# Performance work log

Measured on AMD Instinct MI355X. Metric: run time of the kernel, lower is better.

Reference implementation:

```python
import jax, jax.numpy as jnp
import numpy as np

K = 1024
HEADS = 16


def setup_inputs() -> dict:
    key = jax.random.key(0)
    ks = jax.random.split(key, 6)
    x = jax.random.normal(ks[0], (2, 2048, K), dtype=jnp.float32)
    sc = 1.0 / np.sqrt(K)
    Wq = jax.random.normal(ks[1], (K, K), dtype=jnp.float32) * sc
    Wk = jax.random.normal(ks[2], (K, K), dtype=jnp.float32) * sc
    Wv = jax.random.normal(ks[3], (K, K), dtype=jnp.float32) * sc
    Wu = jax.random.normal(ks[4], (K, K), dtype=jnp.float32) * sc
    bu = jax.random.normal(ks[5], (K,), dtype=jnp.float32) * 0.01
    return {"x": x, "Wq": Wq, "Wk": Wk, "Wv": Wv, "Wu": Wu, "bu": bu}


def reference(x, Wq, Wk, Wv, Wu, bu):
    b, t, k = x.shape
    h = HEADS
    s = k // h
    # torch Linear: y = x @ W.T
    q = (x @ Wq.T).reshape(b, t, h, s)
    kk = (x @ Wk.T).reshape(b, t, h, s)
    v = (x @ Wv.T).reshape(b, t, h, s)
    # NOTE: original scales by sqrt(k) (full model dim), not sqrt(head dim)
    dot = jnp.einsum('bqhs,bkhs->bhqk', q, kk) / jnp.sqrt(jnp.float32(k))
    attn = jax.nn.softmax(dot, axis=-1)
    out = jnp.einsum('bhqk,bkhs->bqhs', attn, v).reshape(b, t, k)
    return out @ Wu.T + bu
```

## Files before the change

kernel.cpp:

```cpp
#include <hip/hip_runtime.h>
#include <hip/hip_bf16.h>


typedef __bf16 bf16x8 __attribute__((ext_vector_type(8)));
typedef float f32x4 __attribute__((ext_vector_type(4)));
typedef float f32x16 __attribute__((ext_vector_type(16)));
typedef unsigned int u32x4 __attribute__((ext_vector_type(4)));

static __device__ __forceinline__ unsigned short f2bf(float f) {
  union { float f; unsigned u; } a; a.f = f;
  unsigned r = a.u + 0x7fff + ((a.u >> 16) & 1);
  return (unsigned short)(r >> 16);
}

static __device__ __forceinline__ unsigned cvt_pk_bf16(float lo, float hi) {
  unsigned r;
  asm("v_cvt_pk_bf16_f32 %0, %1, %2" : "=v"(r) : "v"(lo), "v"(hi));
  return r;
}

static __device__ __forceinline__ float fexp2(float x) {
#if __has_builtin(__builtin_amdgcn_exp2f)
  return __builtin_amdgcn_exp2f(x);
#else
  float r; asm("v_exp_f32 %0, %1\n\ts_nop 0" : "=v"(r) : "v"(x)); return r;
#endif
}

static __device__ __forceinline__ void swap32(unsigned a, unsigned b,
                                              unsigned& x, unsigned& y, int hi) {
#if __has_builtin(__builtin_amdgcn_permlane32_swap)
  typedef unsigned u32x2 __attribute__((ext_vector_type(2)));
  u32x2 r = __builtin_amdgcn_permlane32_swap(a, b, false, false);
  x = r.x; y = r.y;
#else
  unsigned pa = (unsigned)__shfl_xor((int)a, 32, 64);
  unsigned pb = (unsigned)__shfl_xor((int)b, 32, 64);
  x = hi ? pb : a;
  y = hi ? b : pa;
#endif
}

static __device__ __forceinline__ void gload_lds16(const unsigned short* g, unsigned short* l) {
  __builtin_amdgcn_global_load_lds((const __attribute__((address_space(1))) void*)g,
                                   (__attribute__((address_space(3))) void*)l, 16, 0, 0);
}

static __device__ __forceinline__ float tsum16(const f32x16& v) {
  float a0 = v[0]+v[1], a1 = v[2]+v[3], a2 = v[4]+v[5], a3 = v[6]+v[7];
  float a4 = v[8]+v[9], a5 = v[10]+v[11], a6 = v[12]+v[13], a7 = v[14]+v[15];
  float b0 = a0+a1, b1 = a2+a3, b2 = a4+a5, b3 = a6+a7;
  return (b0+b1) + (b2+b3);
}

__global__ __launch_bounds__(256)
void cast_all(const float* __restrict__ x, const float* __restrict__ wq,
              const float* __restrict__ wk, const float* __restrict__ wv,
              const float* __restrict__ wu,
              unsigned short* __restrict__ xb, unsigned short* __restrict__ wqb,
              unsigned short* __restrict__ wkb, unsigned short* __restrict__ wvb,
              unsigned short* __restrict__ wub)
{
  int bid = blockIdx.x;
  const float* src; unsigned short* dst; int blk;
  if (bid < 4096)      { src = x;  dst = xb;  blk = bid; }
  else if (bid < 5120) { src = wq; dst = wqb; blk = bid - 4096; }
  else if (bid < 6144) { src = wk; dst = wkb; blk = bid - 5120; }
  else if (bid < 7168) { src = wv; dst = wvb; blk = bid - 6144; }
  else                 { src = wu; dst = wub; blk = bid - 7168; }
  int idx = blk * 1024 + threadIdx.x * 4;
  float4 v = *(const float4*)&src[idx];
  ushort4 o;
  o.x = f2bf(v.x); o.y = f2bf(v.y); o.z = f2bf(v.z); o.w = f2bf(v.w);
  *(ushort4*)&dst[idx] = o;
}

__global__ __launch_bounds__(512, 2)
void gemm_qkv(const unsigned short* __restrict__ A,
              const unsigned short* __restrict__ Bq,
              const unsigned short* __restrict__ Bk,
              const unsigned short* __restrict__ Bv,
              unsigned short* __restrict__ Qo,
              unsigned short* __restrict__ Ko,
              unsigned short* __restrict__ Vo)
{
  const int Ksz = 1024;
  __shared__ __align__(16) unsigned short As[128 * 32];
  __shared__ __align__(16) unsigned short Bs[128 * 32];
  const int z = blockIdx.z;
  const unsigned short* B = (z == 0) ? Bq : (z == 1) ? Bk : Bv;
  const int tid  = threadIdx.x;
  const int lane = tid & 63;
  const int wid  = tid >> 6;
  const int wr   = wid >> 2, wc = wid & 3;
  const int g    = lane >> 4, r = lane & 15;
  const int bm   = blockIdx.x * 128, bn = blockIdx.y * 128;

  f32x4 acc[4][2] = {};

  const int grow = lane >> 2;
  const int gcol = (lane & 3) * 8;
  const unsigned short* Ag = &A[(size_t)(bm + wid*16 + grow) * Ksz + gcol];
  const unsigned short* Bg = &B[(size_t)(bn + wid*16 + grow) * Ksz + gcol];
  unsigned short* AsW = &As[wid * 512];
  unsigned short* BsW = &Bs[wid * 512];

  for (int k0 = 0; k0 < Ksz; k0 += 32) {
    __syncthreads();
    gload_lds16(Ag + k0, AsW);
    gload_lds16(Bg + k0, BsW);
    __syncthreads();
    bf16x8 af[4], bfr[2];
#pragma unroll
    for (int mi = 0; mi < 4; ++mi)
      af[mi] = *(const bf16x8*)&As[(wr*64 + mi*16 + r) * 32 + g*8];
#pragma unroll
    for (int ni = 0; ni < 2; ++ni)
      bfr[ni] = *(const bf16x8*)&Bs[(wc*32 + ni*16 + r) * 32 + g*8];
#pragma unroll
    for (int mi = 0; mi < 4; ++mi)
#pragma unroll
      for (int ni = 0; ni < 2; ++ni)
        acc[mi][ni] = __builtin_amdgcn_mfma_f32_16x16x32_bf16(af[mi], bfr[ni], acc[mi][ni], 0, 0, 0);
  }

  const float scale = (z == 0) ? (0.03125f * 1.4426950408889634f) : 1.0f;
#pragma unroll
  for (int mi = 0; mi < 4; ++mi)
#pragma unroll
    for (int ni = 0; ni < 2; ++ni) {
      if (z == 2) {
        int m0 = bm + wr*64 + mi*16 + g*4;
        int n  = bn + wc*32 + ni*16 + r;
        int b = m0 >> 11, t0 = m0 & 2047;
        int h = n >> 6,  s = n & 63;
        ushort4 o;
        o.x = f2bf(acc[mi][ni][0]); o.y = f2bf(acc[mi][ni][1]);
        o.z = f2bf(acc[mi][ni][2]); o.w = f2bf(acc[mi][ni][3]);
        *(ushort4*)&Vo[((size_t)((b*16 + h)*64 + s)) * 2048 + t0] = o;
      } else {
        unsigned short* dst = (z == 0) ? Qo : Ko;
#pragma unroll
        for (int q = 0; q < 4; ++q) {
          int m = bm + wr*64 + mi*16 + g*4 + q;
          int n = bn + wc*32 + ni*16 + r;
          int b = m >> 11, t = m & 2047;
          int h = n >> 6,  s = n & 63;
          dst[((size_t)((b*16 + h)*2048 + t)) * 64 + s] = f2bf(acc[mi][ni][q] * scale);
        }
      }
    }
}

__global__ __launch_bounds__(512, 2)
void gemm_final(const unsigned short* __restrict__ A,
                const unsigned short* __restrict__ B,
                float* __restrict__ Cf,
                const float* __restrict__ bias)
{
  const int Ksz = 1024, N = 1024;
  __shared__ __align__(16) unsigned short As[128 * 32];
  __shared__ __align__(16) unsigned short Bs[128 * 32];
  const int tid  = threadIdx.x;
  const int lane = tid & 63;
  const int wid  = tid >> 6;
  const int wr   = wid >> 2, wc = wid & 3;
  const int g    = lane >> 4, r = lane & 15;
  const int bm   = blockIdx.x * 128, bn = blockIdx.y * 128;

  f32x4 acc[4][2] = {};

  const int grow = lane >> 2;
  const int gcol = (lane & 3) * 8;
  const unsigned short* Ag = &A[(size_t)(bm + wid*16 + grow) * Ksz + gcol];
  const unsigned short* Bg = &B[(size_t)(bn + wid*16 + grow) * Ksz + gcol];
  unsigned short* AsW = &As[wid * 512];
  unsigned short* BsW = &Bs[wid * 512];

  for (int k0 = 0; k0 < Ksz; k0 += 32) {
    __syncthreads();
    gload_lds16(Ag + k0, AsW);
    gload_lds16(Bg + k0, BsW);
    __syncthreads();
    bf16x8 af[4], bfr[2];
#pragma unroll
    for (int mi = 0; mi < 4; ++mi)
      af[mi] = *(const bf16x8*)&As[(wr*64 + mi*16 + r) * 32 + g*8];
#pragma unroll
    for (int ni = 0; ni < 2; ++ni)
      bfr[ni] = *(const bf16x8*)&Bs[(wc*32 + ni*16 + r) * 32 + g*8];
#pragma unroll
    for (int mi = 0; mi < 4; ++mi)
#pragma unroll
      for (int ni = 0; ni < 2; ++ni)
        acc[mi][ni] = __builtin_amdgcn_mfma_f32_16x16x32_bf16(af[mi], bfr[ni], acc[mi][ni], 0, 0, 0);
  }

#pragma unroll
  for (int mi = 0; mi < 4; ++mi)
#pragma unroll
    for (int ni = 0; ni < 2; ++ni)
#pragma unroll
      for (int q = 0; q < 4; ++q) {
        int m = bm + wr*64 + mi*16 + g*4 + q;
        int n = bn + wc*32 + ni*16 + r;
        Cf[(size_t)m * N + n] = acc[mi][ni][q] + bias[n];
      }
}

__global__ __launch_bounds__(256)
void attn_kernel(const unsigned short* __restrict__ Qg,
                 const unsigned short* __restrict__ Kg,
                 const unsigned short* __restrict__ Vtg,
                 unsigned short* __restrict__ Og)
{
  const int T = 2048;
  __shared__ __align__(16) unsigned short sK[2][128 * 64];
  __shared__ __align__(16) unsigned short sV[2][64 * 128];

  const int tid = threadIdx.x, lane = tid & 63, wid = tid >> 6;
  const int q32 = lane & 31;
  const int kh  = lane >> 5;

  int bid  = blockIdx.x + 16 * blockIdx.y;
  int nb   = (bid & 7) * 64 + (bid >> 3);
  int bh   = nb >> 4;
  int qblk = nb & 15;
  int qbase = qblk * 128 + wid * 32;

  const size_t base = (size_t)bh * T * 64;
  const unsigned short* Qh = Qg + base;
  const unsigned short* Kh = Kg + base;
  const unsigned short* Vh = Vtg + base;

  const int krow_l  = lane >> 3;
  const int kchunk  = (lane & 7) ^ (krow_l & 7);
  const int vrow_l  = lane >> 4;
  const int vchunkp = lane & 15;

  bf16x8 qf[4];
#pragma unroll
  for (int s = 0; s < 4; ++s)
    qf[s] = *(const bf16x8*)&Qh[(size_t)(qbase + q32)*64 + s*16 + kh*8];

  f32x16 oacc[2] = {};
  float l_own = 0.f;

#pragma unroll
  for (int r = 0; r < 4; ++r) {
    int kr = r*32 + wid*8;
    gload_lds16(Kh + (size_t)(kr + krow_l)*64 + kchunk*8, &sK[0][kr*64]);
    int vr = r*16 + wid*4;
    int vrow = vr + vrow_l;
    gload_lds16(Vh + (size_t)vrow*T + ((vchunkp ^ (vrow & 7))*8), &sV[0][vr*128]);
  }
  __syncthreads();

  int buf = 0;
#pragma unroll 1
  for (int t = 0; t < 16; ++t) {
    if (t < 15) {
      const int kv1 = (t + 1) * 128;
#pragma unroll
      for (int r = 0; r < 4; ++r) {
        int kr = r*32 + wid*8;
        gload_lds16(Kh + (size_t)(kv1 + kr + krow_l)*64 + kchunk*8,
                    &sK[buf^1][kr*64]);
        int vr = r*16 + wid*4;
        int vrow = vr + vrow_l;
        gload_lds16(Vh + (size_t)vrow*T + kv1 + ((vchunkp ^ (vrow & 7))*8),
                    &sV[buf^1][vr*128]);
      }
    }

#pragma unroll
    for (int st = 0; st < 4; ++st) {
      f32x16 a = {};
      const int kvr = st*32 + q32;
#pragma unroll
      for (int s = 0; s < 4; ++s) {
        const int c = (s*2 + kh) ^ (kvr & 7);
        bf16x8 kf = *(const bf16x8*)&sK[buf][kvr*64 + c*8];
        a = __builtin_amdgcn_mfma_f32_32x32x16_bf16(kf, qf[s], a, 0, 0, 0);
      }
#pragma unroll
      for (int r = 0; r < 16; ++r)
        a[r] = fexp2(a[r]);
      l_own += tsum16(a);

      unsigned U[8];
#pragma unroll
      for (int i = 0; i < 8; ++i)
        U[i] = cvt_pk_bf16(a[2*i], a[2*i + 1]);
      unsigned w[8];
      swap32(U[0], U[2], w[0], w[2], kh);
      swap32(U[1], U[3], w[1], w[3], kh);
      swap32(U[4], U[6], w[4], w[6], kh);
      swap32(U[5], U[7], w[5], w[7], kh);
#pragma unroll
      for (int c = 0; c < 2; ++c) {
        u32x4 pw = { w[c*4 + 0], w[c*4 + 1], w[c*4 + 2], w[c*4 + 3] };
        bf16x8 pf = __builtin_bit_cast(bf16x8, pw);
#pragma unroll
        for (int mt = 0; mt < 2; ++mt) {
          const int sr = mt*32 + q32;
          const int cc = (st*4 + c*2 + kh) ^ (sr & 7);
          bf16x8 vfr = *(const bf16x8*)&sV[buf][sr*128 + cc*8];
          oacc[mt] = __builtin_amdgcn_mfma_f32_32x32x16_bf16(vfr, pf, oacc[mt], 0, 0, 0);
        }
      }
    }

    __syncthreads();
    buf ^= 1;
  }

  const float l = l_own + __shfl_xor(l_own, 32, 64);
  const int h = bh & 15, b = bh >> 4;
  const float inv = 1.0f / l;
  const int tq = qbase + q32;
#pragma unroll
  for (int mt = 0; mt < 2; ++mt)
#pragma unroll
    for (int rg = 0; rg < 4; ++rg) {
      ushort4 o;
      o.x = f2bf(oacc[mt][rg*4 + 0] * inv);
      o.y = f2bf(oacc[mt][rg*4 + 1] * inv);
      o.z = f2bf(oacc[mt][rg*4 + 2] * inv);
      o.w = f2bf(oacc[mt][rg*4 + 3] * inv);
      int sd = mt*32 + rg*8 + kh*4;
      *(ushort4*)&Og[((size_t)(b*2048 + tq))*1024 + h*64 + sd] = o;
    }
}

extern "C" void kernel_launch(void* const* d_in, const int* in_sizes, int n_in,
                              void* d_out, int out_size, void* d_ws, size_t ws_size,
                              hipStream_t stream) {
  const float* x  = (const float*)d_in[0];
  const float* Wq = (const float*)d_in[1];
  const float* Wk = (const float*)d_in[2];
  const float* Wv = (const float*)d_in[3];
  const float* Wu = (const float*)d_in[4];
  const float* bu = (const float*)d_in[5];
  float* out = (float*)d_out;

  char* ws = (char*)d_ws;
  unsigned short* xb  = (unsigned short*)(ws);
  unsigned short* Wqb = (unsigned short*)(ws + (size_t)( 8<<20));
  unsigned short* Wkb = (unsigned short*)(ws + (size_t)(10<<20));
  unsigned short* Wvb = (unsigned short*)(ws + (size_t)(12<<20));
  unsigned short* Wub = (unsigned short*)(ws + (size_t)(14<<20));
  unsigned short* Qg  = (unsigned short*)(ws + (size_t)(16<<20));
  unsigned short* Kg  = (unsigned short*)(ws + (size_t)(24<<20));
  unsigned short* Vtg = (unsigned short*)(ws + (size_t)(32<<20));
  unsigned short* Ab  = xb;

  cast_all<<<dim3(8192), 256, 0, stream>>>(x, Wq, Wk, Wv, Wu, xb, Wqb, Wkb, Wvb, Wub);

  gemm_qkv<<<dim3(32, 8, 3), 512, 0, stream>>>(xb, Wqb, Wkb, Wvb, Qg, Kg, Vtg);

  attn_kernel<<<dim3(16, 32), 256, 0, stream>>>(Qg, Kg, Vtg, Ab);

  gemm_final<<<dim3(32, 8), 512, 0, stream>>>(Ab, Wub, out, bu);
}
```

Baseline: 114.9 us.

## Split attention over KV halves and merge partial outputs in final GEMM

The attention kernel now splits the 2048-long KV range into two halves across a z grid dimension, giving 1024 blocks instead of 512, with smaller 64-row KV tiles and lower LDS use for higher occupancy. Each half writes unnormalized bf16 partial outputs and row sums. The final projection GEMM merges them while loading A: it adds the two partials, multiplies by the reciprocal of the summed normalizer and stages the result into LDS by hand. This trades the async global-to-LDS path for register loads and adds extra partial traffic plus bf16 rounding of unnormalized sums. The split path runs only when the workspace is at least 48 MB.

```diff
diff --git a/kernel.cpp b/kernel.cpp
--- a/kernel.cpp
+++ b/kernel.cpp
@@ -6,11 +6,16 @@
 typedef float f32x4 __attribute__((ext_vector_type(4)));
 typedef float f32x16 __attribute__((ext_vector_type(16)));
 typedef unsigned int u32x4 __attribute__((ext_vector_type(4)));
+typedef unsigned short u16x8 __attribute__((ext_vector_type(8)));
 
 static __device__ __forceinline__ unsigned short f2bf(float f) {
   union { float f; unsigned u; } a; a.f = f;
   unsigned r = a.u + 0x7fff + ((a.u >> 16) & 1);
   return (unsigned short)(r >> 16);
+}
+
+static __device__ __forceinline__ float bf2f(unsigned short u) {
+  union { unsigned u; float f; } x; x.u = ((unsigned)u) << 16; return x.f;
 }
 
 static __device__ __forceinline__ unsigned cvt_pk_bf16(float lo, float hi) {
@@ -24,6 +29,14 @@
   return __builtin_amdgcn_exp2f(x);
 #else
   float r; asm("v_exp_f32 %0, %1\n\ts_nop 0" : "=v"(r) : "v"(x)); return r;
+#endif
+}
+
+static __device__ __forceinline__ float frcp(float x) {
+#if __has_builtin(__builtin_amdgcn_rcpf)
+  return __builtin_amdgcn_rcpf(x);
+#else
+  return 1.0f / x;
 #endif
 }
 
@@ -152,8 +165,12 @@
     }
 }
 
+template<int MERGE>
 __global__ __launch_bounds__(512, 2)
-void gemm_final(const unsigned short* __restrict__ A,
+void gemm_final(const unsigned short* __restrict__ A0,
+                const unsigned short* __restrict__ A1,
+                const float* __restrict__ L0,
+                const float* __restrict__ L1,
                 const unsigned short* __restrict__ B,
                 float* __restrict__ Cf,
                 const float* __restrict__ bias)
@@ -172,16 +189,51 @@
 
   const int grow = lane >> 2;
   const int gcol = (lane & 3) * 8;
-  const unsigned short* Ag = &A[(size_t)(bm + wid*16 + grow) * Ksz + gcol];
+  const int arow = bm + wid*16 + grow;
+  const int bb = arow >> 11, tt = arow & 2047;
+  const unsigned short* Ag = &A0[(size_t)arow * Ksz + gcol];
   const unsigned short* Bg = &B[(size_t)(bn + wid*16 + grow) * Ksz + gcol];
   unsigned short* AsW = &As[wid * 512];
   unsigned short* BsW = &Bs[wid * 512];
 
+  bf16x8 po0 = {}, po1 = {};
+  float pl = 1.0f;
+  if (MERGE) {
+    po0 = *(const bf16x8*)&A0[(size_t)arow * Ksz + gcol];
+    po1 = *(const bf16x8*)&A1[(size_t)arow * Ksz + gcol];
+    size_t li = ((size_t)(bb*16 + (gcol >> 6))) * 2048 + tt;
+    pl = L0[li] + L1[li];
+  }
+
   for (int k0 = 0; k0 < Ksz; k0 += 32) {
     __syncthreads();
-    gload_lds16(Ag + k0, AsW);
+    if (MERGE) {
+      float inv = frcp(pl);
+      u16x8 a0 = __builtin_bit_cast(u16x8, po0);
+      u16x8 a1 = __builtin_bit_cast(u16x8, po1);
+      unsigned pw[4];
+#pragma unroll
+      for (int i = 0; i < 4; ++i) {
+        float lo = (bf2f(a0[2*i])   + bf2f(a1[2*i]))   * inv;
+        float hi = (bf2f(a0[2*i+1]) + bf2f(a1[2*i+1])) * inv;
+        pw[i] = cvt_pk_bf16(lo, hi);
+      }
+      u32x4 pv = { pw[0], pw[1], pw[2], pw[3] };
+      *(bf16x8*)&As[(wid*16 + grow) * 32 + gcol] = __builtin_bit_cast(bf16x8, pv);
+    } else {
+      gload_lds16(Ag + k0, AsW);
+    }
     gload_lds16(Bg + k0, BsW);
     __syncthreads();
+    if (MERGE) {
+      int kn = k0 + 32;
+      if (kn < Ksz) {
+        po0 = *(const bf16x8*)&A0[(size_t)arow * Ksz + kn + gcol];
+        po1 = *(const bf16x8*)&A1[(size_t)arow * Ksz + kn + gcol];
+        size_t li = ((size_t)(bb*16 + (kn >> 6))) * 2048 + tt;
+        pl = L0[li] + L1[li];
+      }
+    }
     bf16x8 af[4], bfr[2];
 #pragma unroll
     for (int mi = 0; mi < 4; ++mi)
@@ -208,15 +260,19 @@
       }
 }
 
-__global__ __launch_bounds__(256)
+template<int SPLIT>
+__global__ __launch_bounds__(256, 4)
 void attn_kernel(const unsigned short* __restrict__ Qg,
                  const unsigned short* __restrict__ Kg,
                  const unsigned short* __restrict__ Vtg,
-                 unsigned short* __restrict__ Og)
+                 unsigned short* __restrict__ O0,
+                 unsigned short* __restrict__ O1,
+                 float* __restrict__ L0,
+                 float* __restrict__ L1)
 {
   const int T = 2048;
-  __shared__ __align__(16) unsigned short sK[2][128 * 64];
-  __shared__ __align__(16) unsigned short sV[2][64 * 128];
+  __shared__ __align__(16) unsigned short sK[2][64 * 64];
+  __shared__ __align__(16) unsigned short sV[2][64 * 64];
 
   const int tid = threadIdx.x, lane = tid & 63, wid = tid >> 6;
   const int q32 = lane & 31;
@@ -228,15 +284,17 @@
   int qblk = nb & 15;
   int qbase = qblk * 128 + wid * 32;
 
+  const int kvh    = SPLIT ? blockIdx.z : 0;
+  const int kvbase = kvh * 1024;
+  const int NT     = SPLIT ? 16 : 32;
+
   const size_t base = (size_t)bh * T * 64;
   const unsigned short* Qh = Qg + base;
   const unsigned short* Kh = Kg + base;
   const unsigned short* Vh = Vtg + base;
 
-  const int krow_l  = lane >> 3;
-  const int kchunk  = (lane & 7) ^ (krow_l & 7);
-  const int vrow_l  = lane >> 4;
-  const int vchunkp = lane & 15;
+  const int srow   = lane >> 3;
+  const int schunk = (lane & 7) ^ srow;
 
   bf16x8 qf[4];
 #pragma unroll
@@ -247,34 +305,28 @@
   float l_own = 0.f;
 
 #pragma unroll
-  for (int r = 0; r < 4; ++r) {
+  for (int r = 0; r < 2; ++r) {
     int kr = r*32 + wid*8;
-    gload_lds16(Kh + (size_t)(kr + krow_l)*64 + kchunk*8, &sK[0][kr*64]);
-    int vr = r*16 + wid*4;
-    int vrow = vr + vrow_l;
-    gload_lds16(Vh + (size_t)vrow*T + ((vchunkp ^ (vrow & 7))*8), &sV[0][vr*128]);
+    gload_lds16(Kh + (size_t)(kvbase + kr + srow)*64 + schunk*8, &sK[0][kr*64]);
+    gload_lds16(Vh + (size_t)(kr + srow)*T + kvbase + schunk*8,  &sV[0][kr*64]);
   }
   __syncthreads();
 
   int buf = 0;
 #pragma unroll 1
-  for (int t = 0; t < 16; ++t) {
-    if (t < 15) {
-      const int kv1 = (t + 1) * 128;
-#pragma unroll
-      for (int r = 0; r < 4; ++r) {
+  for (int t = 0; t < NT; ++t) {
+    if (t < NT - 1) {
+      const int kv1 = kvbase + (t + 1) * 64;
+#pragma unroll
+      for (int r = 0; r < 2; ++r) {
         int kr = r*32 + wid*8;
-        gload_lds16(Kh + (size_t)(kv1 + kr + krow_l)*64 + kchunk*8,
-                    &sK[buf^1][kr*64]);
-        int vr = r*16 + wid*4;
-        int vrow = vr + vrow_l;
-        gload_lds16(Vh + (size_t)vrow*T + kv1 + ((vchunkp ^ (vrow & 7))*8),
-                    &sV[buf^1][vr*128]);
-      }
-    }
-
-#pragma unroll
-    for (int st = 0; st < 4; ++st) {
+        gload_lds16(Kh + (size_t)(kv1 + kr + srow)*64 + schunk*8, &sK[buf^1][kr*64]);
+        gload_lds16(Vh + (size_t)(kr + srow)*T + kv1 + schunk*8,  &sV[buf^1][kr*64]);
+      }
+    }
+
+#pragma unroll
+    for (int st = 0; st < 2; ++st) {
       f32x16 a = {};
       const int kvr = st*32 + q32;
 #pragma unroll
@@ -305,7 +357,7 @@
         for (int mt = 0; mt < 2; ++mt) {
           const int sr = mt*32 + q32;
           const int cc = (st*4 + c*2 + kh) ^ (sr & 7);
-          bf16x8 vfr = *(const bf16x8*)&sV[buf][sr*128 + cc*8];
+          bf16x8 vfr = *(const bf16x8*)&sV[buf][sr*64 + cc*8];
           oacc[mt] = __builtin_amdgcn_mfma_f32_32x32x16_bf16(vfr, pf, oacc[mt], 0, 0, 0);
         }
       }
@@ -317,20 +369,25 @@
 
   const float l = l_own + __shfl_xor(l_own, 32, 64);
   const int h = bh & 15, b = bh >> 4;
-  const float inv = 1.0f / l;
   const int tq = qbase + q32;
+  const float sc = SPLIT ? 1.0f : frcp(l);
+  unsigned short* Od = (SPLIT && kvh) ? O1 : O0;
 #pragma unroll
   for (int mt = 0; mt < 2; ++mt)
 #pragma unroll
     for (int rg = 0; rg < 4; ++rg) {
       ushort4 o;
-      o.x = f2bf(oacc[mt][rg*4 + 0] * inv);
-      o.y = f2bf(oacc[mt][rg*4 + 1] * inv);
-      o.z = f2bf(oacc[mt][rg*4 + 2] * inv);
-      o.w = f2bf(oacc[mt][rg*4 + 3] * inv);
+      o.x = f2bf(oacc[mt][rg*4 + 0] * sc);
+      o.y = f2bf(oacc[mt][rg*4 + 1] * sc);
+      o.z = f2bf(oacc[mt][rg*4 + 2] * sc);
+      o.w = f2bf(oacc[mt][rg*4 + 3] * sc);
       int sd = mt*32 + rg*8 + kh*4;
-      *(ushort4*)&Og[((size_t)(b*2048 + tq))*1024 + h*64 + sd] = o;
-    }
+      *(ushort4*)&Od[((size_t)(b*2048 + tq))*1024 + h*64 + sd] = o;
+    }
+  if (SPLIT && kh == 0) {
+    float* Ld = kvh ? L1 : L0;
+    Ld[(size_t)bh * 2048 + tq] = l;
+  }
 }
 
 extern "C" void kernel_launch(void* const* d_in, const int* in_sizes, int n_in,
@@ -353,13 +410,22 @@
   unsigned short* Qg  = (unsigned short*)(ws + (size_t)(16<<20));
   unsigned short* Kg  = (unsigned short*)(ws + (size_t)(24<<20));
   unsigned short* Vtg = (unsigned short*)(ws + (size_t)(32<<20));
-  unsigned short* Ab  = xb;
+  unsigned short* O0  = xb;
+  unsigned short* O1  = (unsigned short*)(ws + (size_t)(40<<20));
+  float* L0 = (float*)(ws + (size_t)(8<<20));
+  float* L1 = L0 + 32 * 2048;
+
+  const bool split = ws_size >= ((size_t)48 << 20);
 
   cast_all<<<dim3(8192), 256, 0, stream>>>(x, Wq, Wk, Wv, Wu, xb, Wqb, Wkb, Wvb, Wub);
 
   gemm_qkv<<<dim3(32, 8, 3), 512, 0, stream>>>(xb, Wqb, Wkb, Wvb, Qg, Kg, Vtg);
 
-  attn_kernel<<<dim3(16, 32), 256, 0, stream>>>(Qg, Kg, Vtg, Ab);
-
-  gemm_final<<<dim3(32, 8), 512, 0, stream>>>(Ab, Wub, out, bu);
-}
+  if (split) {
+    attn_kernel<1><<<dim3(16, 32, 2), 256, 0, stream>>>(Qg, Kg, Vtg, O0, O1, L0, L1);
+    gemm_final<1><<<dim3(32, 8), 512, 0, stream>>>(O0, O1, L0, L1, Wub, out, bu);
+  } else {
+    attn_kernel<0><<<dim3(16, 32, 1), 256, 0, stream>>>(Qg, Kg, Vtg, O0, O0, L0, L0);
+    gemm_final<0><<<dim3(32, 8), 512, 0, stream>>>(O0, O0, L0, L0, Wub, out, bu);
+  }
+}
```

Measured after the change: 128.3 us. 11.6% more time.
